# Kernel optimization log

Hardware: AMD Instinct MI355X
Metric: run time of the kernel (lower is better)

## Reference

```python
import jax, jax.numpy as jnp
import numpy as np

D_MODEL = 1024
NUM_HEADS = 16
THETA = 10000.0
BATCH = 2
SEQ = 2048


def setup_inputs() -> dict:
    key = jax.random.key(0)
    ks = jax.random.split(key, 5)
    std = (2.0 / (D_MODEL + D_MODEL)) ** 0.5
    mk = lambda k: jax.random.truncated_normal(k, -3.0, 3.0, (D_MODEL, D_MODEL), jnp.float32) * std
    return {
        'x': jax.random.normal(ks[0], (BATCH, SEQ, D_MODEL), jnp.float32),
        'Wq': mk(ks[1]),
        'Wk': mk(ks[2]),
        'Wv': mk(ks[3]),
        'Wo': mk(ks[4]),
        'token_positions': jnp.arange(SEQ, dtype=jnp.int32),
    }


def _apply_rope(x, token_positions, theta):
    # x: (B, H, S, d_k)
    d_k = x.shape[-1]
    freq = 1.0 / theta ** (jnp.arange(0, d_k, 2, dtype=jnp.float32) / d_k)  # (d_k//2,)
    freqs = token_positions.astype(jnp.float32)[:, None] * freq[None, :]   # (S, d_k//2)
    cos, sin = jnp.cos(freqs), jnp.sin(freqs)
    x_real = x[..., 0::2]
    x_imag = x[..., 1::2]
    rot_real = x_real * cos - x_imag * sin
    rot_imag = x_real * sin + x_imag * cos
    # interleave back: (..., d_k//2, 2) -> (..., d_k)
    out = jnp.stack([rot_real, rot_imag], axis=-1)
    return out.reshape(x.shape)


def reference(x, Wq, Wk, Wv, Wo, token_positions):
    B, S, D = x.shape
    H = NUM_HEADS
    d_k = D // H

    def split_heads(t):
        return t.reshape(B, S, H, d_k).transpose(0, 2, 1, 3)  # (B, H, S, d_k)

    Q = split_heads(jnp.einsum('bsd,od->bso', x, Wq))
    K = split_heads(jnp.einsum('bsd,od->bso', x, Wk))
    V = split_heads(jnp.einsum('bsd,od->bso', x, Wv))

    Q = _apply_rope(Q, token_positions, THETA)
    K = _apply_rope(K, token_positions, THETA)

    # naive materialized attention with causal mask, faithful to source
    scores = jnp.einsum('bhqd,bhkd->bhqk', Q, K)
    causal = jnp.tril(jnp.ones((S, S), dtype=bool))  # True = attend
    scores = jnp.where(causal[None, None], scores, -jnp.inf)
    scores = scores / jnp.sqrt(jnp.asarray(d_k, scores.dtype))
    probs = jax.nn.softmax(scores, axis=-1)
    attn = jnp.einsum('bhqk,bhkd->bhqd', probs, V)  # (B, H, S, d_v)

    attn = attn.transpose(0, 2, 1, 3).reshape(B, S, D)
    return jnp.einsum('bsd,od->bso', attn, Wo)
```

## Files before the change

### kernel.cpp

```cpp
#include <hip/hip_runtime.h>
#include <hip/hip_bf16.h>
#include <math.h>

#define NUM_HEADS 16
#define DK 64
#define SEQ 2048
#define BATCHN 2
#define DM 1024
#define BS (BATCHN*SEQ)
#define LSCALE 0.18033688011112042f

typedef __bf16 bf16x8 __attribute__((ext_vector_type(8)));
typedef float floatx4 __attribute__((ext_vector_type(4)));
typedef unsigned short ushort;
typedef unsigned int uint;

__device__ __forceinline__ ushort f2bu(float f){
    union { __hip_bfloat16 h; ushort u; } cv; cv.h = __float2bfloat16(f); return cv.u;
}
__device__ __forceinline__ uint packbf(float a, float b){
    return (uint)f2bu(a) | ((uint)f2bu(b) << 16);
}
__device__ __forceinline__ float bu2f(ushort u){
    union { uint u; float f; } cv; cv.u = (uint)u << 16; return cv.f;
}
__device__ __forceinline__ uint cvtpk(float lo, float hi){
    uint r; asm("v_cvt_pk_bf16_f32 %0, %1, %2" : "=v"(r) : "v"(lo), "v"(hi));
    return r;
}
__device__ __forceinline__ void gl16(const void* g, void* l){
    __builtin_amdgcn_global_load_lds(
        (const __attribute__((address_space(1))) unsigned int*)g,
        (__attribute__((address_space(3))) unsigned int*)l, 16, 0, 0);
}

__global__ __launch_bounds__(256)
void castall(const float* __restrict__ x,  const float* __restrict__ wq,
             const float* __restrict__ wk, const float* __restrict__ wv,
             const float* __restrict__ wo, const int* __restrict__ pos,
             ushort* __restrict__ xb, ushort* __restrict__ wqkb,
             ushort* __restrict__ wvb, ushort* __restrict__ wob,
             float2* __restrict__ tab)
{
    int bid = blockIdx.x;
    if (bid >= 4096) {
        int idx = (bid - 4096)*256 + threadIdx.x;
        int s = idx >> 5, i = idx & 31;
        float invf = expf(-0.28782313662425575f * (float)i);
        float ang = (float)pos[s] * invf;
        float sn, cs; sincosf(ang, &sn, &cs);
        tab[idx] = make_float2(cs, sn);
        return;
    }
    const float* src; ushort* dst; int off;
    if (bid < 2048)      { src = x;  dst = xb;             off = bid; }
    else if (bid < 2560) { src = wq; dst = wqkb;           off = bid - 2048; }
    else if (bid < 3072) { src = wk; dst = wqkb + 1048576; off = bid - 2560; }
    else if (bid < 3584) { src = wv; dst = wvb;            off = bid - 3072; }
    else                 { src = wo; dst = wob;            off = bid - 3584; }
    int i = off*2048 + threadIdx.x*8;
    float4 a = *(const float4*)(src+i);
    float4 b = *(const float4*)(src+i+4);
    uint4 o;
    o.x = packbf(a.x, a.y);
    o.y = packbf(a.z, a.w);
    o.z = packbf(b.x, b.y);
    o.w = packbf(b.z, b.w);
    *(uint4*)(dst+i) = o;
}

__global__ __launch_bounds__(256)
void proj_fused(const ushort* __restrict__ xb, const ushort* __restrict__ Wqkb,
                const ushort* __restrict__ Wvb, ushort* __restrict__ Qb,
                ushort* __restrict__ VTp, const float2* __restrict__ rope)
{
    __shared__ ushort As[2*128*32];
    __shared__ ushort Bs[2*128*32];

    const int bid = blockIdx.x;
    const ushort* A; const ushort* W; int row0, col0, mode;
    if (bid < 512) { A = xb;  W = Wqkb; row0 = (bid >> 4) * 128;
                     col0 = (bid & 15) * 128;  mode = 1; }
    else           { int i = bid - 512; A = Wvb; W = xb;
                     row0 = (i >> 5) * 128; col0 = (i & 31) * 128; mode = 2; }

    const int t = threadIdx.x;
    const int w = t >> 6;
    const int L = t & 63;
    const int lr = L & 15;
    const int lq = L >> 4;
    const int wrow = w * 32;

    floatx4 acc[2][8];
    #pragma unroll
    for (int i = 0; i < 2; ++i)
        #pragma unroll
        for (int j = 0; j < 8; ++j)
            acc[i][j] = (floatx4){0.f,0.f,0.f,0.f};

    const int rr = t >> 2, cb = t & 3;
    const int ko = (cb ^ ((rr >> 1) & 3)) * 8;
    const int ldst = rr*32 + cb*8;
    const ushort* ga = A + (size_t)(row0 + rr) * DM + ko;
    const ushort* gb = W + (size_t)(col0 + rr) * DM + ko;

    const int co = (lq*8) ^ (((lr >> 1) & 3) << 3);

#define STG(BUF, K0)                                                          \
    {                                                                         \
        gl16(ga + (K0),                 &As[(BUF)*4096 + ldst]);              \
        gl16(ga + (K0) + (size_t)64*DM, &As[(BUF)*4096 + 2048 + ldst]);       \
        gl16(gb + (K0),                 &Bs[(BUF)*4096 + ldst]);              \
        gl16(gb + (K0) + (size_t)64*DM, &Bs[(BUF)*4096 + 2048 + ldst]);       \
    }

    STG(0, 0)
    asm volatile("s_waitcnt vmcnt(0)" ::: "memory");
    __builtin_amdgcn_sched_barrier(0);
    __builtin_amdgcn_s_barrier();

    int cur = 0;
    for (int k0 = 0; k0 < DM; k0 += 32) {
        const int nxt = cur ^ 1;
        if (k0 + 32 < DM) STG(nxt, k0 + 32)
        const ushort* Ac = As + cur*4096;
        const ushort* Bc = Bs + cur*4096;
        bf16x8 aF0 = *(const bf16x8*)&Ac[(wrow + lr)*32 + co];
        bf16x8 aF1 = *(const bf16x8*)&Ac[(wrow + 16 + lr)*32 + co];
        #pragma unroll
        for (int tc = 0; tc < 8; ++tc) {
            bf16x8 bF = *(const bf16x8*)&Bc[(tc*16 + lr)*32 + co];
            acc[0][tc] = __builtin_amdgcn_mfma_f32_16x16x32_bf16(aF0, bF, acc[0][tc], 0, 0, 0);
            acc[1][tc] = __builtin_amdgcn_mfma_f32_16x16x32_bf16(aF1, bF, acc[1][tc], 0, 0, 0);
        }
        asm volatile("s_waitcnt vmcnt(0) lgkmcnt(0)" ::: "memory");
        __builtin_amdgcn_sched_barrier(0);
        __builtin_amdgcn_s_barrier();
        cur = nxt;
    }
#undef STG

    if (mode == 2) {
        #pragma unroll
        for (int tr = 0; tr < 2; ++tr)
            #pragma unroll
            for (int tc = 0; tc < 8; ++tc)
                #pragma unroll
                for (int r = 0; r < 4; ++r) {
                    int m = row0 + wrow + tr*16 + lq*4 + r;
                    int c = col0 + tc*16 + lr;
                    VTp[(size_t)m * BS + c] = f2bu(acc[tr][tc][r]);
                }
    } else {
        const int mat = col0 >> 10;
        const int base_hh = (col0 & 1023) >> 6;
        ushort* out = Qb + (size_t)mat * (BATCHN*NUM_HEADS*SEQ*DK);
        const float qscale = mat ? 1.f : LSCALE;
        #pragma unroll
        for (int tr = 0; tr < 2; ++tr)
            #pragma unroll
            for (int tc = 0; tc < 8; ++tc)
                #pragma unroll
                for (int r = 0; r < 4; ++r) {
                    int m = row0 + wrow + tr*16 + lq*4 + r;
                    int b = m >> 11;
                    int s = m & (SEQ - 1);
                    int dd = (tc*16 + lr) & 63;
                    int hh = base_hh + (tc >> 2);
                    float v = acc[tr][tc][r];
                    float o = __shfl_xor(v, 1, 64);
                    float2 cs = rope[s*32 + (dd >> 1)];
                    float rv = (dd & 1) ? fmaf(o, cs.y,  v * cs.x)
                                        : fmaf(-o, cs.y, v * cs.x);
                    out[((size_t)((b*NUM_HEADS + hh)*SEQ + s))*DK + dd] =
                        f2bu(rv * qscale);
                }
    }
}

__global__ __launch_bounds__(256)
void gemm_out(const ushort* __restrict__ A, const ushort* __restrict__ W,
              float* __restrict__ out)
{
    __shared__ ushort As[2*128*32];
    __shared__ ushort Bs[2*64*32];

    const int t = threadIdx.x;
    const int w = t >> 6;
    const int L = t & 63;
    const int lr = L & 15;
    const int lq = L >> 4;
    const int row0 = blockIdx.y * 128;
    const int col0 = blockIdx.x * 64;
    const int wrow = w * 32;

    floatx4 acc[2][4];
    #pragma unroll
    for (int i = 0; i < 2; ++i)
        #pragma unroll
        for (int j = 0; j < 4; ++j)
            acc[i][j] = (floatx4){0.f,0.f,0.f,0.f};

    const int rr = t >> 2, cb = t & 3;
    const int ko = (cb ^ ((rr >> 1) & 3)) * 8;
    const int ldst = rr*32 + cb*8;
    const ushort* ga = A + (size_t)(row0 + rr) * DM + ko;
    const ushort* gb = W + (size_t)(col0 + rr) * DM + ko;

    const int co = (lq*8) ^ (((lr >> 1) & 3) << 3);

#define STG(BUF, K0)                                                          \
    {                                                                         \
        gl16(ga + (K0),                 &As[(BUF)*4096 + ldst]);              \
        gl16(ga + (K0) + (size_t)64*DM, &As[(BUF)*4096 + 2048 + ldst]);       \
        gl16(gb + (K0),                 &Bs[(BUF)*2048 + ldst]);              \
    }

    STG(0, 0)
    asm volatile("s_waitcnt vmcnt(0)" ::: "memory");
    __builtin_amdgcn_sched_barrier(0);
    __builtin_amdgcn_s_barrier();

    int cur = 0;
    for (int k0 = 0; k0 < DM; k0 += 32) {
        const int nxt = cur ^ 1;
        if (k0 + 32 < DM) STG(nxt, k0 + 32)
        const ushort* Ac = As + cur*4096;
        const ushort* Bc = Bs + cur*2048;
        bf16x8 aF0 = *(const bf16x8*)&Ac[(wrow + lr)*32 + co];
        bf16x8 aF1 = *(const bf16x8*)&Ac[(wrow + 16 + lr)*32 + co];
        #pragma unroll
        for (int tc = 0; tc < 4; ++tc) {
            bf16x8 bF = *(const bf16x8*)&Bc[(tc*16 + lr)*32 + co];
            acc[0][tc] = __builtin_amdgcn_mfma_f32_16x16x32_bf16(aF0, bF, acc[0][tc], 0, 0, 0);
            acc[1][tc] = __builtin_amdgcn_mfma_f32_16x16x32_bf16(aF1, bF, acc[1][tc], 0, 0, 0);
        }
        asm volatile("s_waitcnt vmcnt(0) lgkmcnt(0)" ::: "memory");
        __builtin_amdgcn_sched_barrier(0);
        __builtin_amdgcn_s_barrier();
        cur = nxt;
    }
#undef STG

    #pragma unroll
    for (int tr = 0; tr < 2; ++tr)
        #pragma unroll
        for (int tc = 0; tc < 4; ++tc)
            #pragma unroll
            for (int r = 0; r < 4; ++r) {
                int m = row0 + wrow + tr*16 + lq*4 + r;
                int c = col0 + tc*16 + lr;
                out[(size_t)m * DM + c] = acc[tr][tc][r];
            }
}

__global__ __launch_bounds__(128)
void attn_mfma(const ushort* __restrict__ Qb, const ushort* __restrict__ Kb,
               const ushort* __restrict__ VT, ushort* __restrict__ attnb,
               ushort* __restrict__ Opart, float* __restrict__ lpart)
{
    __shared__ ushort Ks[64*64];
    __shared__ ushort Vs[64*64];

    const int t = threadIdx.x;
    const int w = t >> 6;
    const int L = t & 63;
    const int lr = L & 15, lq = L >> 4;
    const int h  = blockIdx.y;
    const int b  = blockIdx.z;

    int qt, chunk, nch;
    {
        const int bx = blockIdx.x;
        if (bx < 8)       { qt = bx;              chunk = 0;     nch = 1; }
        else if (bx < 24) { int i = bx - 8;  qt = 8  + (i>>1); chunk = i&1;        nch = 2; }
        else if (bx < 48) { int i = bx - 24; int q3 = i/3; qt = 16 + q3; chunk = i - q3*3; nch = 3; }
        else              { int i = bx - 48; qt = 24 + (i>>2); chunk = i&3;        nch = 4; }
    }
    const int nt = qt + 1;
    const int t0 = (nt * chunk) / nch;
    const int t1 = (nt * (chunk + 1)) / nch;
    const int q0 = qt * 64;
    const int qw = q0 + w * 32;
    const size_t qkbase = (size_t)(b*NUM_HEADS + h) * SEQ * DK;

    bf16x8 qA0, qA1, qB0, qB1;
    {
        const ushort* qp = Qb + qkbase + (size_t)(qw + lr) * DK + lq*8;
        qA0 = *(const bf16x8*)qp;
        qA1 = *(const bf16x8*)(qp + 32);
        qB0 = *(const bf16x8*)(qp + 16*DK);
        qB1 = *(const bf16x8*)(qp + 16*DK + 32);
    }

    bf16x8 ones8;
    {
        union { uint u[4]; bf16x8 v; } o;
        o.u[0] = o.u[1] = o.u[2] = o.u[3] = 0x3f803f80u;
        ones8 = o.v;
    }

    floatx4 O0[4], O1[4];
    #pragma unroll
    for (int g = 0; g < 4; ++g) {
        O0[g] = (floatx4){0.f,0.f,0.f,0.f};
        O1[g] = (floatx4){0.f,0.f,0.f,0.f};
    }
    floatx4 lA = (floatx4){0.f,0.f,0.f,0.f};
    floatx4 lB = (floatx4){0.f,0.f,0.f,0.f};

    const int sr = t >> 3, t7 = t & 7;
    const int kwb  = (sr*64 + t7*8) ^ ((sr & 7) << 3);
    const int pc0  = ((t7 >> 2) << 3) | ((t7 & 1) << 2) | ((t7 >> 1) & 1);
    const int vwb0 = (sr*64 + pc0*4)     ^ ((sr & 7) << 3);
    const int vwb1 = (sr*64 + pc0*4 + 8) ^ ((sr & 7) << 3);
    const ushort* kpt = Kb + qkbase + (size_t)sr * DK + t7*8;
    const ushort* vpt = VT + ((size_t)(h*DK + sr)) * BS + b*SEQ + t7*8;

    const int kro0 = (lr*64 + lq*8)      ^ ((lr & 7) << 3);
    const int kro1 = (lr*64 + 32 + lq*8) ^ ((lr & 7) << 3);

    uint4 kv0, kv1, kv2, kv3, vv0, vv1, vv2, vv3;

#define GLOAD(T)                                                              \
    {                                                                         \
        const ushort* kg = kpt + (size_t)(T) * 64 * DK;                       \
        const ushort* vg = vpt + (T) * 64;                                    \
        kv0 = *(const uint4*)(kg);                                            \
        kv1 = *(const uint4*)(kg + 16*DK);                                    \
        kv2 = *(const uint4*)(kg + 32*DK);                                    \
        kv3 = *(const uint4*)(kg + 48*DK);                                    \
        vv0 = *(const uint4*)(vg);                                            \
        vv1 = *(const uint4*)(vg + (size_t)16*BS);                            \
        vv2 = *(const uint4*)(vg + (size_t)32*BS);                            \
        vv3 = *(const uint4*)(vg + (size_t)48*BS);                            \
    }

#define STAGE()                                                               \
    {                                                                         \
        *(uint4*)&Ks[kwb]        = kv0;                                       \
        *(uint4*)&Ks[kwb + 1024] = kv1;                                       \
        *(uint4*)&Ks[kwb + 2048] = kv2;                                       \
        *(uint4*)&Ks[kwb + 3072] = kv3;                                       \
        *(uint2*)&Vs[vwb0]        = make_uint2(vv0.x, vv0.y);                 \
        *(uint2*)&Vs[vwb1]        = make_uint2(vv0.z, vv0.w);                 \
        *(uint2*)&Vs[vwb0 + 1024] = make_uint2(vv1.x, vv1.y);                 \
        *(uint2*)&Vs[vwb1 + 1024] = make_uint2(vv1.z, vv1.w);                 \
        *(uint2*)&Vs[vwb0 + 2048] = make_uint2(vv2.x, vv2.y);                 \
        *(uint2*)&Vs[vwb1 + 2048] = make_uint2(vv2.z, vv2.w);                 \
        *(uint2*)&Vs[vwb0 + 3072] = make_uint2(vv3.x, vv3.y);                 \
        *(uint2*)&Vs[vwb1 + 3072] = make_uint2(vv3.z, vv3.w);                 \
    }

#define COMPUTE(LASTT)                                                        \
    {                                                                         \
        uint2 pk0[4], pk1[4];                                                 \
        _Pragma("unroll")                                                     \
        for (int g = 0; g < 4; ++g) {                                         \
            bf16x8 kf0 = *(const bf16x8*)&Ks[kro0 + g*1024];                  \
            bf16x8 kf1 = *(const bf16x8*)&Ks[kro1 + g*1024];                  \
            floatx4 s0 = (floatx4){0.f,0.f,0.f,0.f};                          \
            s0 = __builtin_amdgcn_mfma_f32_16x16x32_bf16(kf0, qA0, s0,0,0,0); \
            s0 = __builtin_amdgcn_mfma_f32_16x16x32_bf16(kf1, qA1, s0,0,0,0); \
            floatx4 s1 = (floatx4){0.f,0.f,0.f,0.f};                          \
            s1 = __builtin_amdgcn_mfma_f32_16x16x32_bf16(kf0, qB0, s1,0,0,0); \
            s1 = __builtin_amdgcn_mfma_f32_16x16x32_bf16(kf1, qB1, s1,0,0,0); \
            float a0 = __builtin_amdgcn_exp2f(s0[0]);                         \
            float a1 = __builtin_amdgcn_exp2f(s0[1]);                         \
            float a2 = __builtin_amdgcn_exp2f(s0[2]);                         \
            float a3 = __builtin_amdgcn_exp2f(s0[3]);                         \
            float b0 = __builtin_amdgcn_exp2f(s1[0]);                         \
            float b1 = __builtin_amdgcn_exp2f(s1[1]);                         \
            float b2 = __builtin_amdgcn_exp2f(s1[2]);                         \
            float b3 = __builtin_amdgcn_exp2f(s1[3]);                         \
            if (LASTT) {                                                      \
                const int kbase = g*16 + lq*4;                                \
                a0 = (kbase + 0 <= lim0) ? a0 : 0.f;                          \
                a1 = (kbase + 1 <= lim0) ? a1 : 0.f;                          \
                a2 = (kbase + 2 <= lim0) ? a2 : 0.f;                          \
                a3 = (kbase + 3 <= lim0) ? a3 : 0.f;                          \
                b0 = (kbase + 0 <= lim1) ? b0 : 0.f;                          \
                b1 = (kbase + 1 <= lim1) ? b1 : 0.f;                          \
                b2 = (kbase + 2 <= lim1) ? b2 : 0.f;                          \
                b3 = (kbase + 3 <= lim1) ? b3 : 0.f;                          \
            }                                                                 \
            pk0[g] = make_uint2(cvtpk(a0, a1), cvtpk(a2, a3));                \
            pk1[g] = make_uint2(cvtpk(b0, b1), cvtpk(b2, b3));                \
        }                                                                     \
        _Pragma("unroll")                                                     \
        for (int c = 0; c < 2; ++c) {                                         \
            union { uint u[4]; bf16x8 v; } a0u, a1u;                          \
            a0u.u[0] = pk0[2*c].x;   a0u.u[1] = pk0[2*c].y;                   \
            a0u.u[2] = pk0[2*c+1].x; a0u.u[3] = pk0[2*c+1].y;                 \
            a1u.u[0] = pk1[2*c].x;   a1u.u[1] = pk1[2*c].y;                   \
            a1u.u[2] = pk1[2*c+1].x; a1u.u[3] = pk1[2*c+1].y;                 \
            lA = __builtin_amdgcn_mfma_f32_16x16x32_bf16(a0u.v, ones8, lA,0,0,0); \
            lB = __builtin_amdgcn_mfma_f32_16x16x32_bf16(a1u.v, ones8, lB,0,0,0); \
            const int vro = c ? kro1 : kro0;                                  \
            _Pragma("unroll")                                                 \
            for (int g2 = 0; g2 < 4; ++g2) {                                  \
                bf16x8 vf = *(const bf16x8*)&Vs[vro + g2*1024];               \
                O0[g2] = __builtin_amdgcn_mfma_f32_16x16x32_bf16(a0u.v, vf, O0[g2],0,0,0); \
                O1[g2] = __builtin_amdgcn_mfma_f32_16x16x32_bf16(a1u.v, vf, O1[g2],0,0,0); \
            }                                                                 \
        }                                                                     \
    }

    GLOAD(t0);
    const bool haslast = (t1 == nt);
    const int tmain = haslast ? t1 - 1 : t1;
    {
        const int lim0 = 0, lim1 = 0;
        for (int tile = t0; tile < tmain; ++tile) {
            __syncthreads();
            STAGE();
            __syncthreads();
            if (tile + 1 < t1) GLOAD(tile + 1);
            COMPUTE(false);
        }
    }
    if (haslast) {
        __syncthreads();
        STAGE();
        __syncthreads();
        const int lim0 = qw + lr - (nt - 1)*64;
        const int lim1 = lim0 + 16;
        COMPUTE(true);
    }
#undef GLOAD
#undef STAGE
#undef COMPUTE

    if (nch == 1) {
        #pragma unroll
        for (int r = 0; r < 4; ++r) {
            float li0 = 1.f / lA[r];
            float li1 = 1.f / lB[r];
            int s0r = qw + lq*4 + r;
            int s1r = qw + 16 + lq*4 + r;
            #pragma unroll
            for (int g2 = 0; g2 < 4; ++g2) {
                attnb[((size_t)(b*SEQ + s0r))*DM + h*DK + g2*16 + lr] = f2bu(O0[g2][r] * li0);
                attnb[((size_t)(b*SEQ + s1r))*DM + h*DK + g2*16 + lr] = f2bu(O1[g2][r] * li1);
            }
        }
    } else {
        const int slot = ((b*NUM_HEADS + h)*24 + (qt - 8))*4 + chunk;
        ushort* Op = Opart + (size_t)slot * 4096;
        #pragma unroll
        for (int r = 0; r < 4; ++r) {
            int ql0 = w*32 + lq*4 + r;
            int ql1 = w*32 + 16 + lq*4 + r;
            #pragma unroll
            for (int g2 = 0; g2 < 4; ++g2) {
                Op[ql0*64 + g2*16 + lr] = f2bu(O0[g2][r]);
                Op[ql1*64 + g2*16 + lr] = f2bu(O1[g2][r]);
            }
        }
        if (lr == 0) {
            #pragma unroll
            for (int r = 0; r < 4; ++r) {
                lpart[(size_t)slot*64 + w*32 + lq*4 + r]      = lA[r];
                lpart[(size_t)slot*64 + w*32 + 16 + lq*4 + r] = lB[r];
            }
        }
    }
}

__global__ __launch_bounds__(256)
void combine(const ushort* __restrict__ Opart, const float* __restrict__ lpart,
             ushort* __restrict__ attnb)
{
    int gx = blockIdx.x;
    int qti = gx % 24, bh = gx / 24;
    int h = bh & 15, b = bh >> 4;
    int qt = 8 + qti;
    int nch = (qt >> 3) + 1;
    int tid = threadIdx.x;
    int row = tid >> 2, c0 = (tid & 3) * 16;
    const int base_slot = (bh*24 + qti)*4;

    float acc[16];
    #pragma unroll
    for (int e = 0; e < 16; ++e) acc[e] = 0.f;
    float l = 0.f;

    for (int c = 0; c < nch; ++c) {
        const ushort* Op = Opart + (size_t)(base_slot + c)*4096 + row*64 + c0;
        uint4 u0 = *(const uint4*)(Op);
        uint4 u1 = *(const uint4*)(Op + 8);
        const ushort* h0 = (const ushort*)&u0;
        const ushort* h1 = (const ushort*)&u1;
        #pragma unroll
        for (int e = 0; e < 8; ++e) { acc[e]   += bu2f(h0[e]); }
        #pragma unroll
        for (int e = 0; e < 8; ++e) { acc[8+e] += bu2f(h1[e]); }
        l += lpart[(size_t)(base_slot + c)*64 + row];
    }
    float li = 1.f / l;
    int s = qt*64 + row;
    ushort* dst = attnb + ((size_t)(b*SEQ + s))*DM + h*DK + c0;
    #pragma unroll
    for (int e = 0; e < 16; ++e) dst[e] = f2bu(acc[e] * li);
}

extern "C" void kernel_launch(void* const* d_in, const int* in_sizes, int n_in,
                              void* d_out, int out_size, void* d_ws, size_t ws_size,
                              hipStream_t stream) {
    const float* x   = (const float*)d_in[0];
    const float* Wq  = (const float*)d_in[1];
    const float* Wk  = (const float*)d_in[2];
    const float* Wv  = (const float*)d_in[3];
    const float* Wo  = (const float*)d_in[4];
    const int*   pos = (const int*)d_in[5];
    float* out = (float*)d_out;

    const size_t MB = 1u << 20;
    char* ws = (char*)d_ws;
    ushort* xb    = (ushort*)(ws);
    ushort* Wqkb  = (ushort*)(ws +  8*MB);
    ushort* Wvb   = (ushort*)(ws + 12*MB);
    ushort* Opart = (ushort*)(ws);
    float*  lpart = (float*)(ws + 24*MB);
    ushort* Qb    = (ushort*)(ws + 25*MB);
    ushort* Kb    = (ushort*)(ws + 33*MB);
    ushort* VT    = (ushort*)(ws + 41*MB);
    ushort* attnb = (ushort*)(ws + 49*MB);
    float2* ropeT = (float2*)(ws + 57*MB);
    ushort* Wob   = (ushort*)(ws + 58*MB);

    dim3 blk(256);
    castall<<<4352, blk, 0, stream>>>(x, Wq, Wk, Wv, Wo, pos,
                                      xb, Wqkb, Wvb, Wob, ropeT);

    proj_fused<<<768, blk, 0, stream>>>(xb, Wqkb, Wvb, Qb, VT, ropeT);

    attn_mfma<<<dim3(80, NUM_HEADS, BATCHN), dim3(128), 0, stream>>>(Qb, Kb, VT, attnb,
                                                                     Opart, lpart);
    combine<<<768, blk, 0, stream>>>(Opart, lpart, attnb);

    gemm_out<<<dim3(16,32), blk, 0, stream>>>(attnb, Wob, out);
}
```

Before: 194.4 us.

## Split-K output GEMM with atomics, simplify projection GEMM to single-buffer LDS

The output GEMM is split along K into two halves, doubling the block count to 1024, and the partial sums are accumulated into the output with float atomic adds. The output buffer is zeroed in extra blocks of the cast kernel. The output GEMM's pipeline waits are relaxed to vmcnt(3) so the next tile's loads overlap the current compute. Separately, the projection GEMM drops its double-buffered, XOR-swizzled LDS staging for a plain single buffer with two __syncthreads per K step, which exposes load latency and risks LDS bank conflicts.

```diff
diff --git a/kernel.cpp b/kernel.cpp
--- a/kernel.cpp
+++ b/kernel.cpp
@@ -40,9 +40,16 @@
              const float* __restrict__ wo, const int* __restrict__ pos,
              ushort* __restrict__ xb, ushort* __restrict__ wqkb,
              ushort* __restrict__ wvb, ushort* __restrict__ wob,
-             float2* __restrict__ tab)
+             float2* __restrict__ tab, float* __restrict__ outz)
 {
     int bid = blockIdx.x;
+    if (bid >= 4352) {
+        int fi = (bid - 4352)*8192 + threadIdx.x*8;
+        float4 z = make_float4(0.f, 0.f, 0.f, 0.f);
+        *(float4*)(outz + fi)     = z;
+        *(float4*)(outz + fi + 4) = z;
+        return;
+    }
     if (bid >= 4096) {
         int idx = (bid - 4096)*256 + threadIdx.x;
         int s = idx >> 5, i = idx & 31;
@@ -74,8 +81,8 @@
                 const ushort* __restrict__ Wvb, ushort* __restrict__ Qb,
                 ushort* __restrict__ VTp, const float2* __restrict__ rope)
 {
-    __shared__ ushort As[2*128*32];
-    __shared__ ushort Bs[2*128*32];
+    __shared__ ushort As[128][32];
+    __shared__ ushort Bs[128][32];
 
     const int bid = blockIdx.x;
     const ushort* A; const ushort* W; int row0, col0, mode;
@@ -98,47 +105,27 @@
         for (int j = 0; j < 8; ++j)
             acc[i][j] = (floatx4){0.f,0.f,0.f,0.f};
 
-    const int rr = t >> 2, cb = t & 3;
-    const int ko = (cb ^ ((rr >> 1) & 3)) * 8;
-    const int ldst = rr*32 + cb*8;
+    const int rr = t >> 2, ko = (t & 3) * 8;
     const ushort* ga = A + (size_t)(row0 + rr) * DM + ko;
     const ushort* gb = W + (size_t)(col0 + rr) * DM + ko;
 
-    const int co = (lq*8) ^ (((lr >> 1) & 3) << 3);
-
-#define STG(BUF, K0)                                                          \
-    {                                                                         \
-        gl16(ga + (K0),                 &As[(BUF)*4096 + ldst]);              \
-        gl16(ga + (K0) + (size_t)64*DM, &As[(BUF)*4096 + 2048 + ldst]);       \
-        gl16(gb + (K0),                 &Bs[(BUF)*4096 + ldst]);              \
-        gl16(gb + (K0) + (size_t)64*DM, &Bs[(BUF)*4096 + 2048 + ldst]);       \
-    }
-
-    STG(0, 0)
-    asm volatile("s_waitcnt vmcnt(0)" ::: "memory");
-    __builtin_amdgcn_sched_barrier(0);
-    __builtin_amdgcn_s_barrier();
-
-    int cur = 0;
     for (int k0 = 0; k0 < DM; k0 += 32) {
-        const int nxt = cur ^ 1;
-        if (k0 + 32 < DM) STG(nxt, k0 + 32)
-        const ushort* Ac = As + cur*4096;
-        const ushort* Bc = Bs + cur*4096;
-        bf16x8 aF0 = *(const bf16x8*)&Ac[(wrow + lr)*32 + co];
-        bf16x8 aF1 = *(const bf16x8*)&Ac[(wrow + 16 + lr)*32 + co];
+        __syncthreads();
+        gl16(ga + k0,                    &As[rr][ko]);
+        gl16(ga + k0 + (size_t)64*DM,    &As[rr + 64][ko]);
+        gl16(gb + k0,                    &Bs[rr][ko]);
+        gl16(gb + k0 + (size_t)64*DM,    &Bs[rr + 64][ko]);
+        __syncthreads();
+
+        bf16x8 aF0 = *(const bf16x8*)&As[wrow + lr][lq*8];
+        bf16x8 aF1 = *(const bf16x8*)&As[wrow + 16 + lr][lq*8];
         #pragma unroll
         for (int tc = 0; tc < 8; ++tc) {
-            bf16x8 bF = *(const bf16x8*)&Bc[(tc*16 + lr)*32 + co];
+            bf16x8 bF = *(const bf16x8*)&Bs[tc*16 + lr][lq*8];
             acc[0][tc] = __builtin_amdgcn_mfma_f32_16x16x32_bf16(aF0, bF, acc[0][tc], 0, 0, 0);
             acc[1][tc] = __builtin_amdgcn_mfma_f32_16x16x32_bf16(aF1, bF, acc[1][tc], 0, 0, 0);
         }
-        asm volatile("s_waitcnt vmcnt(0) lgkmcnt(0)" ::: "memory");
-        __builtin_amdgcn_sched_barrier(0);
-        __builtin_amdgcn_s_barrier();
-        cur = nxt;
-    }
-#undef STG
+    }
 
     if (mode == 2) {
         #pragma unroll
@@ -185,13 +172,18 @@
     __shared__ ushort As[2*128*32];
     __shared__ ushort Bs[2*64*32];
 
+    const int bid = blockIdx.x;
+    const int tb  = bid & 511;
+    const int kh  = bid >> 9;
+    const int row0 = (tb >> 4) * 128;
+    const int col0 = (tb & 15) * 64;
+    const int kbase = kh * 512;
+
     const int t = threadIdx.x;
     const int w = t >> 6;
     const int L = t & 63;
     const int lr = L & 15;
     const int lq = L >> 4;
-    const int row0 = blockIdx.y * 128;
-    const int col0 = blockIdx.x * 64;
     const int wrow = w * 32;
 
     floatx4 acc[2][4];
@@ -204,8 +196,8 @@
     const int rr = t >> 2, cb = t & 3;
     const int ko = (cb ^ ((rr >> 1) & 3)) * 8;
     const int ldst = rr*32 + cb*8;
-    const ushort* ga = A + (size_t)(row0 + rr) * DM + ko;
-    const ushort* gb = W + (size_t)(col0 + rr) * DM + ko;
+    const ushort* ga = A + (size_t)(row0 + rr) * DM + kbase + ko;
+    const ushort* gb = W + (size_t)(col0 + rr) * DM + kbase + ko;
 
     const int co = (lq*8) ^ (((lr >> 1) & 3) << 3);
 
@@ -217,14 +209,20 @@
     }
 
     STG(0, 0)
-    asm volatile("s_waitcnt vmcnt(0)" ::: "memory");
-    __builtin_amdgcn_sched_barrier(0);
-    __builtin_amdgcn_s_barrier();
 
     int cur = 0;
-    for (int k0 = 0; k0 < DM; k0 += 32) {
+    for (int k0 = 0; k0 < 512; k0 += 32) {
         const int nxt = cur ^ 1;
-        if (k0 + 32 < DM) STG(nxt, k0 + 32)
+        if (k0 + 32 < 512) {
+            STG(nxt, k0 + 32)
+            asm volatile("s_waitcnt vmcnt(3)" ::: "memory");
+        } else {
+            asm volatile("s_waitcnt vmcnt(0)" ::: "memory");
+        }
+        __builtin_amdgcn_sched_barrier(0);
+        __builtin_amdgcn_s_barrier();
+        __builtin_amdgcn_sched_barrier(0);
+
         const ushort* Ac = As + cur*4096;
         const ushort* Bc = Bs + cur*2048;
         bf16x8 aF0 = *(const bf16x8*)&Ac[(wrow + lr)*32 + co];
@@ -235,9 +233,10 @@
             acc[0][tc] = __builtin_amdgcn_mfma_f32_16x16x32_bf16(aF0, bF, acc[0][tc], 0, 0, 0);
             acc[1][tc] = __builtin_amdgcn_mfma_f32_16x16x32_bf16(aF1, bF, acc[1][tc], 0, 0, 0);
         }
-        asm volatile("s_waitcnt vmcnt(0) lgkmcnt(0)" ::: "memory");
+        asm volatile("s_waitcnt lgkmcnt(0)" ::: "memory");
         __builtin_amdgcn_sched_barrier(0);
         __builtin_amdgcn_s_barrier();
+        __builtin_amdgcn_sched_barrier(0);
         cur = nxt;
     }
 #undef STG
@@ -250,7 +249,7 @@
             for (int r = 0; r < 4; ++r) {
                 int m = row0 + wrow + tr*16 + lq*4 + r;
                 int c = col0 + tc*16 + lr;
-                out[(size_t)m * DM + c] = acc[tr][tc][r];
+                unsafeAtomicAdd(out + (size_t)m * DM + c, acc[tr][tc][r]);
             }
 }
 
@@ -530,8 +529,8 @@
     ushort* Wob   = (ushort*)(ws + 58*MB);
 
     dim3 blk(256);
-    castall<<<4352, blk, 0, stream>>>(x, Wq, Wk, Wv, Wo, pos,
-                                      xb, Wqkb, Wvb, Wob, ropeT);
+    castall<<<4864, blk, 0, stream>>>(x, Wq, Wk, Wv, Wo, pos,
+                                      xb, Wqkb, Wvb, Wob, ropeT, out);
 
     proj_fused<<<768, blk, 0, stream>>>(xb, Wqkb, Wvb, Qb, VT, ropeT);
 
@@ -539,5 +538,5 @@
                                                                      Opart, lpart);
     combine<<<768, blk, 0, stream>>>(Opart, lpart, attnb);
 
-    gemm_out<<<dim3(16,32), blk, 0, stream>>>(attnb, Wob, out);
-}
+    gemm_out<<<1024, blk, 0, stream>>>(attnb, Wob, out);
+}
```

Result: slower. 212.2 us (+9.2%).
